# Performance work log

Hardware: AMD Instinct MI355X
Metric: run time of the kernel (lower is better)

The kernel has to match this reference:

```python
import jax, jax.numpy as jnp
import numpy as np

NUM_NODES = 100000
NUM_EDGES = 625000
IN_FEATURES = 128
OUT_FEATURES = 128


def setup_inputs() -> dict:
    key = jax.random.key(0)
    k1, k2, k3, k4 = jax.random.split(key, 4)
    x = jax.random.normal(k1, (NUM_NODES, IN_FEATURES), dtype=jnp.float32)
    edge_index = jax.random.randint(k2, (2, NUM_EDGES), 0, NUM_NODES, dtype=jnp.int64)
    # Xavier uniform for W (fan_in=IN, fan_out=OUT); B initialized to zeros in the
    # original, but we use small random values so gradients flow through both paths.
    limit = float(np.sqrt(6.0 / (IN_FEATURES + OUT_FEATURES)))
    W = jax.random.uniform(k3, (OUT_FEATURES, IN_FEATURES), dtype=jnp.float32,
                           minval=-limit, maxval=limit)
    B = jax.random.uniform(k4, (OUT_FEATURES, IN_FEATURES), dtype=jnp.float32,
                           minval=-limit, maxval=limit)
    return {"x": x, "edge_index": edge_index, "W": W, "B": B}


def reference(x, edge_index, W, B):
    sources, destinations = edge_index[0], edge_index[1]
    # message: gather destination features, scatter-add into source slots
    messages = x[destinations]                                        # [E, F_in]
    agg = jax.ops.segment_sum(messages, sources, num_segments=x.shape[0])  # [N, F_in]
    # in-degree (w.r.t. sources) normalization; zero-degree -> divide by 1
    deg = jax.ops.segment_sum(jnp.ones((sources.shape[0],), dtype=x.dtype),
                              sources, num_segments=x.shape[0])       # [N]
    deg = jnp.where(deg == 0, jnp.ones_like(deg), deg)
    agg = agg / deg[:, None]
    # update: (W @ messages.T + B @ x.T).T == messages @ W.T + x @ B.T
    out = agg @ W.T + x @ B.T                                         # [N, F_out]
    return out
```

## Files before the change

kernel.cpp:

```cpp
#include <hip/hip_runtime.h>

#define F_IN   128
#define F_OUT  128

typedef __attribute__((ext_vector_type(8))) short short8;
typedef __attribute__((ext_vector_type(4))) float floatx4;

__device__ __forceinline__ float bf16u_to_f_lo(unsigned int u) {
    union { unsigned int i; float f; } c; c.i = u << 16; return c.f;
}
__device__ __forceinline__ float bf16u_to_f_hi(unsigned int u) {
    union { unsigned int i; float f; } c; c.i = u & 0xffff0000u; return c.f;
}
__device__ __forceinline__ unsigned short f_to_bf16(float f) {
    union { float f; unsigned int i; } c; c.f = f;
    unsigned int u = c.i;
    u += 0x7fffu + ((u >> 16) & 1u);
    return (unsigned short)(u >> 16);
}
__device__ __forceinline__ unsigned int pack2(unsigned short a, unsigned short b) {
    return (unsigned int)a | ((unsigned int)b << 16);
}

__device__ __forceinline__ void gload_lds16(const void* g, void* l) {
    __builtin_amdgcn_global_load_lds(
        (const __attribute__((address_space(1))) unsigned int*)g,
        (__attribute__((address_space(3))) unsigned int*)l, 16, 0, 0);
}

__global__ __launch_bounds__(256) void init_kernel(const float* __restrict__ x,
                                                   char* __restrict__ outb,
                                                   const float* __restrict__ W,
                                                   const float* __restrict__ Bm,
                                                   uint4* __restrict__ bfrag,
                                                   int* __restrict__ btot,
                                                   const int* __restrict__ ei,
                                                   int N, int E, int nbconv, int nbhist) {
    int b = blockIdx.x;
    int t = threadIdx.x;
    if (b < nbconv) {
        long tid = (long)b * 256 + t;
        if (tid < (long)N * 32) {
            int row = (int)(tid >> 5);
            int seg = (int)(tid & 31);
            float4 v = *(const float4*)(x + (size_t)row * 128 + seg * 4);
            unsigned short r[4] = {f_to_bf16(v.x), f_to_bf16(v.y), f_to_bf16(v.z), f_to_bf16(v.w)};
            *(ushort4*)(outb + (size_t)row * 512 + 256 + seg * 8) =
                make_ushort4(r[0], r[1], r[2], r[3]);
        }
        return;
    }
    if (b < nbconv + nbhist) {
        __shared__ int h[256];
        h[t] = 0;
        __syncthreads();
        int e0 = (b - nbconv) * 1024;
#pragma unroll
        for (int j = 0; j < 4; ++j) {
            int idx = e0 + j * 256 + t;
            if (idx < E) atomicAdd(&h[ei[idx] >> 9], 1);
        }
        __syncthreads();
        if (h[t]) atomicAdd(&btot[t], h[t]);
        return;
    }
#pragma unroll
    for (int i = 0; i < 16; ++i) {
        int flat = i * 256 + t;
        int lane = flat & 63;
        int idx = flat >> 6;
        int nt = idx >> 3, sfrag = idx & 7;
        int n = nt * 16 + (lane & 15);
        int kbase = sfrag * 32 + (lane >> 4) * 8;
        const float* srcp = (kbase < 128) ? (W + n * 128 + kbase)
                                          : (Bm + n * 128 + (kbase - 128));
        float4 v0 = *(const float4*)srcp;
        float4 v1 = *(const float4*)(srcp + 4);
        uint4 pk;
        pk.x = pack2(f_to_bf16(v0.x), f_to_bf16(v0.y));
        pk.y = pack2(f_to_bf16(v0.z), f_to_bf16(v0.w));
        pk.z = pack2(f_to_bf16(v1.x), f_to_bf16(v1.y));
        pk.w = pack2(f_to_bf16(v1.z), f_to_bf16(v1.w));
        bfrag[flat] = pk;
    }
}

__global__ __launch_bounds__(256) void scan256_kernel(const int* __restrict__ btot,
                                                      int* __restrict__ gbase,
                                                      int* __restrict__ gcur, int NB) {
    __shared__ int s[256];
    int t = threadIdx.x;
    s[t] = (t < NB) ? btot[t] : 0;
    __syncthreads();
    for (int d = 1; d < 256; d <<= 1) {
        int v = s[t] + ((t >= d) ? s[t - d] : 0);
        __syncthreads();
        s[t] = v;
        __syncthreads();
    }
    int excl = (t > 0) ? s[t - 1] : 0;
    if (t < NB) { gbase[t] = excl; gcur[t] = excl; }
    if (t == 0) gbase[NB] = s[255];
}

__global__ __launch_bounds__(256) void pass1_kernel(const int* __restrict__ ei,
                                                    int* __restrict__ gcur,
                                                    int* __restrict__ ebuf, int E) {
    __shared__ int cnt[256];
    __shared__ int base[256];
    __shared__ int cur[256];
    int t = threadIdx.x;
    cnt[t] = 0;
    cur[t] = 0;
    int e0 = blockIdx.x * 1024;
    __syncthreads();
    int s[4];
#pragma unroll
    for (int j = 0; j < 4; ++j) {
        int idx = e0 + j * 256 + t;
        s[j] = (idx < E) ? ei[idx] : -1;
        if (s[j] >= 0) atomicAdd(&cnt[s[j] >> 9], 1);
    }
    __syncthreads();
    int c = cnt[t];
    base[t] = c ? atomicAdd(&gcur[t], c) : 0;
    __syncthreads();
#pragma unroll
    for (int j = 0; j < 4; ++j) {
        if (s[j] >= 0) {
            int idx = e0 + j * 256 + t;
            int bkt = s[j] >> 9;
            int r = atomicAdd(&cur[bkt], 1);
            int d = ei[E + idx];
            ebuf[base[bkt] + r] = ((s[j] & 511) << 17) | d;
        }
    }
}

__global__ __launch_bounds__(256) void pass2_kernel(const int* __restrict__ ebuf,
                                                    const int* __restrict__ gbase,
                                                    int* __restrict__ off,
                                                    int* __restrict__ dst_sorted,
                                                    int N, int NB) {
    __shared__ int sc[512];
    __shared__ int cur[512];
    int g = blockIdx.x, t = threadIdx.x;
    int lo = g << 9;
    int hi = min(N, lo + 512);
    int start = gbase[g];
    int end = gbase[g + 1];
    sc[t] = 0;
    sc[t + 256] = 0;
    __syncthreads();
    for (int i = start + t; i < end; i += 256) atomicAdd(&sc[ebuf[i] >> 17], 1);
    __syncthreads();
    for (int d = 1; d < 512; d <<= 1) {
        int v0 = sc[t] + ((t >= d) ? sc[t - d] : 0);
        int i1 = t + 256;
        int v1 = sc[i1] + sc[i1 - d];
        __syncthreads();
        sc[t] = v0;
        sc[i1] = v1;
        __syncthreads();
    }
    if (lo + t < hi) off[lo + t] = start + sc[t];
    cur[t] = (t == 0) ? 0 : sc[t - 1];
    {
        int i1 = t + 256;
        if (lo + i1 < hi) off[lo + i1] = start + sc[i1];
        cur[i1] = sc[i1 - 1];
    }
    __syncthreads();
    for (int i = start + t; i < end; i += 256) {
        int v = ebuf[i];
        int n = v >> 17;
        int r = atomicAdd(&cur[n], 1);
        dst_sorted[start + r] = v & 0x1FFFF;
    }
}

__global__ __launch_bounds__(256) void gather_bf16_kernel(const int* __restrict__ off,
                                                          const int* __restrict__ dst_sorted,
                                                          char* __restrict__ outb, int N) {
    int node = blockIdx.x * 16 + (threadIdx.x >> 4);
    int lane = threadIdx.x & 15;
    if (node >= N) return;
    int start = (node == 0) ? 0 : off[node - 1];
    int end = off[node];
    float acc[8];
#pragma unroll
    for (int i = 0; i < 8; ++i) acc[i] = 0.0f;

    const char* xb = outb;
    for (int j = start; j < end; j += 8) {
        uint4 v[8];
#pragma unroll
        for (int i = 0; i < 8; ++i) {
            int idx = j + i;
            int clamped = (idx < end) ? idx : (end - 1);
            int d = dst_sorted[clamped];
            v[i] = *(const uint4*)(xb + (size_t)d * 512 + 256 + lane * 16);
        }
#pragma unroll
        for (int i = 0; i < 8; ++i) {
            if (j + i >= end) v[i] = make_uint4(0u, 0u, 0u, 0u);
            acc[0] += bf16u_to_f_lo(v[i].x); acc[1] += bf16u_to_f_hi(v[i].x);
            acc[2] += bf16u_to_f_lo(v[i].y); acc[3] += bf16u_to_f_hi(v[i].y);
            acc[4] += bf16u_to_f_lo(v[i].z); acc[5] += bf16u_to_f_hi(v[i].z);
            acc[6] += bf16u_to_f_lo(v[i].w); acc[7] += bf16u_to_f_hi(v[i].w);
        }
    }
    int deg = end - start;
    float scale = (deg > 0) ? (1.0f / (float)deg) : 1.0f;
    unsigned short r[8];
#pragma unroll
    for (int i = 0; i < 8; ++i) r[i] = f_to_bf16(acc[i] * scale);
    uint4 pk;
    pk.x = pack2(r[0], r[1]);
    pk.y = pack2(r[2], r[3]);
    pk.z = pack2(r[4], r[5]);
    pk.w = pack2(r[6], r[7]);
    *(uint4*)(outb + (size_t)node * 512 + lane * 16) = pk;
}

__global__ __launch_bounds__(256, 2) void gemm_mfma_kernel(const uint4* __restrict__ bfrag,
                                                           float* __restrict__ out, int N) {
    __shared__ uint4 Bs[4096];
    int t = threadIdx.x;
    int lane = t & 63;
    int w = t >> 6;
    int m16 = lane & 15;
    int quad = lane >> 4;

#pragma unroll
    for (int j = 0; j < 16; ++j)
        gload_lds16(bfrag + (w * 16 + j) * 64 + lane, &Bs[(w * 16 + j) * 64]);

    int rowbase = blockIdx.x * 128 + w * 32;
    short8 afrag[2][8];
#pragma unroll
    for (int g = 0; g < 2; ++g) {
        int arow = rowbase + g * 16 + m16;
        if (arow > N - 1) arow = N - 1;
        const char* ab = (const char*)out + (size_t)arow * 512;
#pragma unroll
        for (int s = 0; s < 8; ++s)
            afrag[g][s] = *(const short8*)(ab + s * 64 + quad * 16);
    }
    __syncthreads();

    floatx4 acc[2][8];
#pragma unroll
    for (int g = 0; g < 2; ++g)
#pragma unroll
        for (int nt = 0; nt < 8; ++nt) acc[g][nt] = (floatx4){0.f, 0.f, 0.f, 0.f};

#pragma unroll
    for (int nt = 0; nt < 8; ++nt) {
#pragma unroll
        for (int s = 0; s < 8; ++s) {
            short8 bf = *(const short8*)&Bs[(nt * 8 + s) * 64 + lane];
            acc[0][nt] = __builtin_amdgcn_mfma_f32_16x16x32_bf16(afrag[0][s], bf, acc[0][nt], 0, 0, 0);
            acc[1][nt] = __builtin_amdgcn_mfma_f32_16x16x32_bf16(afrag[1][s], bf, acc[1][nt], 0, 0, 0);
        }
    }

#pragma unroll
    for (int g = 0; g < 2; ++g)
#pragma unroll
        for (int nt = 0; nt < 8; ++nt)
#pragma unroll
            for (int r = 0; r < 4; ++r) {
                int gr = rowbase + g * 16 + quad * 4 + r;
                if (gr < N) out[(size_t)gr * 128 + nt * 16 + m16] = acc[g][nt][r];
            }
}

__global__ void zero_kernel(int* __restrict__ p, long n) {
    long i = (long)blockIdx.x * blockDim.x + threadIdx.x;
    long stride = (long)gridDim.x * blockDim.x;
    for (; i < n; i += stride) p[i] = 0;
}

__global__ void invdeg_kernel(int* __restrict__ deg_io, int N) {
    int i = blockIdx.x * blockDim.x + threadIdx.x;
    if (i < N) {
        int d = deg_io[i];
        float inv = (d > 0) ? (1.0f / (float)d) : 1.0f;
        ((float*)deg_io)[i] = inv;
    }
}

__global__ void hist_kernel(const int* __restrict__ src, int* __restrict__ cnt, int E) {
    int e = blockIdx.x * blockDim.x + threadIdx.x;
    if (e < E) atomicAdd(&cnt[src[e]], 1);
}

__global__ __launch_bounds__(128) void scatter_atomic_kernel(const float* __restrict__ x,
                                                             const int* __restrict__ ei,
                                                             const float* __restrict__ invdeg,
                                                             float* __restrict__ out, int E) {
    int e = blockIdx.x;
    int f = threadIdx.x;
    int s = ei[e];
    int d = ei[E + e];
    float v = x[(long)d * F_IN + f] * invdeg[s];
    atomicAdd(&out[(long)s * F_IN + f], v);
}

__global__ __launch_bounds__(256) void gemm_fused_kernel(const float* __restrict__ x,
                                                         const float* __restrict__ W,
                                                         const float* __restrict__ Bm,
                                                         float* __restrict__ out, int N) {
    __shared__ float As[64][68];
    __shared__ float Ms[64][132];
    int t = threadIdx.x;
    int row0 = blockIdx.x * 64;
    int c0 = (t & 31) * 4;
    int r0 = (t >> 5) * 8;
    float acc[8][4];
#pragma unroll
    for (int i = 0; i < 8; ++i)
#pragma unroll
        for (int j = 0; j < 4; ++j) acc[i][j] = 0.0f;

    for (int kc = 0; kc < 4; ++kc) {
        const float* Asrc = (kc < 2) ? out : x;
        const float* Msrc = (kc < 2) ? W : Bm;
        int k0 = (kc & 1) * 64;
#pragma unroll
        for (int i = 0; i < 4; ++i) {
            int flat = t + 256 * i;
            int m = flat >> 4, ks = flat & 15;
            int row = row0 + m;
            float4 v = make_float4(0.f, 0.f, 0.f, 0.f);
            if (row < N) v = *(const float4*)&Asrc[(long)row * 128 + k0 + ks * 4];
            As[ks * 4 + 0][m] = v.x;
            As[ks * 4 + 1][m] = v.y;
            As[ks * 4 + 2][m] = v.z;
            As[ks * 4 + 3][m] = v.w;
        }
#pragma unroll
        for (int i = 0; i < 8; ++i) {
            int flat = t + 256 * i;
            int c = flat >> 4, ks = flat & 15;
            float4 v = *(const float4*)&Msrc[(long)c * 128 + k0 + ks * 4];
            Ms[ks * 4 + 0][c] = v.x;
            Ms[ks * 4 + 1][c] = v.y;
            Ms[ks * 4 + 2][c] = v.z;
            Ms[ks * 4 + 3][c] = v.w;
        }
        __syncthreads();
#pragma unroll 8
        for (int kk = 0; kk < 64; ++kk) {
            float4 a0 = *(const float4*)&As[kk][r0];
            float4 a1 = *(const float4*)&As[kk][r0 + 4];
            float4 m0 = *(const float4*)&Ms[kk][c0];
            float a[8] = {a0.x, a0.y, a0.z, a0.w, a1.x, a1.y, a1.z, a1.w};
            float m[4] = {m0.x, m0.y, m0.z, m0.w};
#pragma unroll
            for (int i = 0; i < 8; ++i)
#pragma unroll
                for (int j = 0; j < 4; ++j) acc[i][j] += a[i] * m[j];
        }
        __syncthreads();
    }
#pragma unroll
    for (int i = 0; i < 8; ++i) {
        int row = row0 + r0 + i;
        if (row < N) {
            float4 v = make_float4(acc[i][0], acc[i][1], acc[i][2], acc[i][3]);
            *(float4*)&out[(long)row * 128 + c0] = v;
        }
    }
}


extern "C" void kernel_launch(void* const* d_in, const int* in_sizes, int n_in,
                              void* d_out, int out_size, void* d_ws, size_t ws_size,
                              hipStream_t stream) {
    const float* x = (const float*)d_in[0];
    const int* ei = (const int*)d_in[1];
    const float* W = (const float*)d_in[2];
    const float* Bm = (const float*)d_in[3];
    float* out = (float*)d_out;

    const int N = in_sizes[0] / F_IN;
    const int E = in_sizes[1] / 2;
    const int NB = (N + 511) >> 9;
    const int nbconv = (int)(((long)N * 32 + 255) / 256);
    const int nbhist = (E + 1023) / 1024;

    const size_t need_main = 4096 * sizeof(uint4) +
                             ((size_t)772 + (size_t)N + 2 * (size_t)E) * sizeof(int);
    const size_t need_deg = (size_t)N * sizeof(int);

    if (ws_size >= need_main && N <= 131072) {
        uint4* bfrag = (uint4*)d_ws;
        int* btot    = (int*)(bfrag + 4096);
        int* gbase   = btot + 256;
        int* gcur    = gbase + 260;
        int* off     = gcur + 256;
        int* ebuf    = off + N;
        int* dst_sorted = ebuf + E;

        hipMemsetAsync(btot, 0, 256 * sizeof(int), stream);
        init_kernel<<<nbconv + nbhist + 1, 256, 0, stream>>>(x, (char*)out, W, Bm,
                                                             bfrag, btot, ei, N, E,
                                                             nbconv, nbhist);
        scan256_kernel<<<1, 256, 0, stream>>>(btot, gbase, gcur, NB);
        pass1_kernel<<<(E + 1023) / 1024, 256, 0, stream>>>(ei, gcur, ebuf, E);
        pass2_kernel<<<NB, 256, 0, stream>>>(ebuf, gbase, off, dst_sorted, N, NB);
        gather_bf16_kernel<<<(N + 15) / 16, 256, 0, stream>>>(off, dst_sorted, (char*)out, N);
        gemm_mfma_kernel<<<(N + 127) / 128, 256, 0, stream>>>(bfrag, out, N);
    } else if (ws_size >= need_deg) {
        int* deg = (int*)d_ws;
        zero_kernel<<<256, 256, 0, stream>>>(deg, N);
        hist_kernel<<<(E + 255) / 256, 256, 0, stream>>>(ei, deg, E);
        invdeg_kernel<<<(N + 255) / 256, 256, 0, stream>>>(deg, N);
        zero_kernel<<<512, 256, 0, stream>>>((int*)out, (long)N * F_IN);
        scatter_atomic_kernel<<<E, 128, 0, stream>>>(x, ei, (const float*)deg, out, E);
        gemm_fused_kernel<<<(N + 63) / 64, 256, 0, stream>>>(x, W, Bm, out, N);
    }
}
```

Baseline: 197.8 us.

## Fold bucket scan into pass kernels and remap gather blocks per XCD

Removes the separate single-block scan kernel by having every pass1 and pass2 block recompute the 256-entry prefix sum of bucket totals in shared memory, with a zeroed per-bucket counter replacing the precomputed cursor. This saves one launch and its serialization at the cost of redundant per-block scan work. The gather kernel's block index is also remapped so that consecutive 128-node tiles land on blocks with the same residue mod 8, presumably to keep each tile's output on one XCD's L2 for the following GEMM.

```diff
diff --git a/kernel.cpp b/kernel.cpp
--- a/kernel.cpp
+++ b/kernel.cpp
@@ -85,35 +85,27 @@
     }
 }
 
-__global__ __launch_bounds__(256) void scan256_kernel(const int* __restrict__ btot,
-                                                      int* __restrict__ gbase,
-                                                      int* __restrict__ gcur, int NB) {
-    __shared__ int s[256];
-    int t = threadIdx.x;
-    s[t] = (t < NB) ? btot[t] : 0;
-    __syncthreads();
-    for (int d = 1; d < 256; d <<= 1) {
-        int v = s[t] + ((t >= d) ? s[t - d] : 0);
-        __syncthreads();
-        s[t] = v;
-        __syncthreads();
-    }
-    int excl = (t > 0) ? s[t - 1] : 0;
-    if (t < NB) { gbase[t] = excl; gcur[t] = excl; }
-    if (t == 0) gbase[NB] = s[255];
-}
-
 __global__ __launch_bounds__(256) void pass1_kernel(const int* __restrict__ ei,
-                                                    int* __restrict__ gcur,
+                                                    const int* __restrict__ btot,
+                                                    int* __restrict__ gcur0,
                                                     int* __restrict__ ebuf, int E) {
+    __shared__ int sc[256];
     __shared__ int cnt[256];
     __shared__ int base[256];
     __shared__ int cur[256];
     int t = threadIdx.x;
+    sc[t] = btot[t];
     cnt[t] = 0;
     cur[t] = 0;
     int e0 = blockIdx.x * 1024;
     __syncthreads();
+    for (int d = 1; d < 256; d <<= 1) {
+        int v = sc[t] + ((t >= d) ? sc[t - d] : 0);
+        __syncthreads();
+        sc[t] = v;
+        __syncthreads();
+    }
+    int gbase_t = (t > 0) ? sc[t - 1] : 0;
     int s[4];
 #pragma unroll
     for (int j = 0; j < 4; ++j) {
@@ -123,7 +115,7 @@
     }
     __syncthreads();
     int c = cnt[t];
-    base[t] = c ? atomicAdd(&gcur[t], c) : 0;
+    base[t] = c ? (gbase_t + atomicAdd(&gcur0[t], c)) : 0;
     __syncthreads();
 #pragma unroll
     for (int j = 0; j < 4; ++j) {
@@ -138,20 +130,28 @@
 }
 
 __global__ __launch_bounds__(256) void pass2_kernel(const int* __restrict__ ebuf,
-                                                    const int* __restrict__ gbase,
+                                                    const int* __restrict__ btot,
                                                     int* __restrict__ off,
                                                     int* __restrict__ dst_sorted,
                                                     int N, int NB) {
+    __shared__ int gb[256];
     __shared__ int sc[512];
     __shared__ int cur[512];
     int g = blockIdx.x, t = threadIdx.x;
     int lo = g << 9;
     int hi = min(N, lo + 512);
-    int start = gbase[g];
-    int end = gbase[g + 1];
+    gb[t] = btot[t];
     sc[t] = 0;
     sc[t + 256] = 0;
     __syncthreads();
+    for (int d = 1; d < 256; d <<= 1) {
+        int v = gb[t] + ((t >= d) ? gb[t - d] : 0);
+        __syncthreads();
+        gb[t] = v;
+        __syncthreads();
+    }
+    int start = (g > 0) ? gb[g - 1] : 0;
+    int end = gb[g];
     for (int i = start + t; i < end; i += 256) atomicAdd(&sc[ebuf[i] >> 17], 1);
     __syncthreads();
     for (int d = 1; d < 512; d <<= 1) {
@@ -182,7 +182,11 @@
 __global__ __launch_bounds__(256) void gather_bf16_kernel(const int* __restrict__ off,
                                                           const int* __restrict__ dst_sorted,
                                                           char* __restrict__ outb, int N) {
-    int node = blockIdx.x * 16 + (threadIdx.x >> 4);
+    int b = blockIdx.x;
+    int r = b & 7, q = b >> 3;
+    int k = q >> 3, s8 = q & 7;
+    int m = r + 8 * k;
+    int node = m * 128 + s8 * 16 + (threadIdx.x >> 4);
     int lane = threadIdx.x & 15;
     if (node >= N) return;
     int start = (node == 0) ? 0 : off[node - 1];
@@ -212,14 +216,14 @@
     }
     int deg = end - start;
     float scale = (deg > 0) ? (1.0f / (float)deg) : 1.0f;
-    unsigned short r[8];
-#pragma unroll
-    for (int i = 0; i < 8; ++i) r[i] = f_to_bf16(acc[i] * scale);
+    unsigned short rr[8];
+#pragma unroll
+    for (int i = 0; i < 8; ++i) rr[i] = f_to_bf16(acc[i] * scale);
     uint4 pk;
-    pk.x = pack2(r[0], r[1]);
-    pk.y = pack2(r[2], r[3]);
-    pk.z = pack2(r[4], r[5]);
-    pk.w = pack2(r[6], r[7]);
+    pk.x = pack2(rr[0], rr[1]);
+    pk.y = pack2(rr[2], rr[3]);
+    pk.z = pack2(rr[4], rr[5]);
+    pk.w = pack2(rr[6], rr[7]);
     *(uint4*)(outb + (size_t)node * 512 + lane * 16) = pk;
 }
 
@@ -390,29 +394,32 @@
     const int NB = (N + 511) >> 9;
     const int nbconv = (int)(((long)N * 32 + 255) / 256);
     const int nbhist = (E + 1023) / 1024;
+    const int ntiles = (N + 127) / 128;
 
     const size_t need_main = 4096 * sizeof(uint4) +
-                             ((size_t)772 + (size_t)N + 2 * (size_t)E) * sizeof(int);
+                             ((size_t)512 + (size_t)N + 2 * (size_t)E) * sizeof(int);
     const size_t need_deg = (size_t)N * sizeof(int);
 
     if (ws_size >= need_main && N <= 131072) {
         uint4* bfrag = (uint4*)d_ws;
         int* btot    = (int*)(bfrag + 4096);
-        int* gbase   = btot + 256;
-        int* gcur    = gbase + 260;
-        int* off     = gcur + 256;
+        int* gcur0   = btot + 256;
+        int* off     = gcur0 + 256;
         int* ebuf    = off + N;
         int* dst_sorted = ebuf + E;
 
-        hipMemsetAsync(btot, 0, 256 * sizeof(int), stream);
+        hipMemsetAsync(btot, 0, 512 * sizeof(int), stream);
         init_kernel<<<nbconv + nbhist + 1, 256, 0, stream>>>(x, (char*)out, W, Bm,
                                                              bfrag, btot, ei, N, E,
                                                              nbconv, nbhist);
-        scan256_kernel<<<1, 256, 0, stream>>>(btot, gbase, gcur, NB);
-        pass1_kernel<<<(E + 1023) / 1024, 256, 0, stream>>>(ei, gcur, ebuf, E);
-        pass2_kernel<<<NB, 256, 0, stream>>>(ebuf, gbase, off, dst_sorted, N, NB);
-        gather_bf16_kernel<<<(N + 15) / 16, 256, 0, stream>>>(off, dst_sorted, (char*)out, N);
-        gemm_mfma_kernel<<<(N + 127) / 128, 256, 0, stream>>>(bfrag, out, N);
+        pass1_kernel<<<(E + 1023) / 1024, 256, 0, stream>>>(ei, btot, gcur0, ebuf, E);
+        pass2_kernel<<<NB, 256, 0, stream>>>(ebuf, btot, off, dst_sorted, N, NB);
+        {
+            int kmax = (ntiles + 7) / 8;
+            int grid = 8 * kmax * 8;
+            gather_bf16_kernel<<<grid, 256, 0, stream>>>(off, dst_sorted, (char*)out, N);
+        }
+        gemm_mfma_kernel<<<ntiles, 256, 0, stream>>>(bfrag, out, N);
     } else if (ws_size >= need_deg) {
         int* deg = (int*)d_ws;
         zero_kernel<<<256, 256, 0, stream>>>(deg, N);
```

Result: faster. 193.0 us (-2.5%).
